# Optimization experiments

Measured on AMD Instinct MI355X. Metric: run time of the kernel, lower is better.

## Reference

```python
import jax, jax.numpy as jnp
import numpy as np

BOUND = 1.0
MIN_NEAR = 0.2
T_THRESH = 1e-4
MAX_STEPS = 128


def _near_far(rays_o, rays_d):
    # ray-AABB intersection with [-BOUND, BOUND]^3 (near_far_from_aabb)
    d = jnp.where(jnp.abs(rays_d) < 1e-9, 1e-9, rays_d)
    t1 = (-BOUND - rays_o) / d
    t2 = (BOUND - rays_o) / d
    near = jnp.max(jnp.minimum(t1, t2), axis=-1)
    far = jnp.min(jnp.maximum(t1, t2), axis=-1)
    near = jnp.maximum(near, MIN_NEAR)
    far = jnp.maximum(far, near)
    return near, far


def _sample_triplane(planes, pts):
    # planes: [3, C, RES, RES]; pts: [N, 3] in [-1, 1] -> feats [N, 3C]
    def bil(plane, uv):
        res = plane.shape[-1]
        xy = (uv + 1.0) * 0.5 * (res - 1)
        x0 = jnp.clip(jnp.floor(xy).astype(jnp.int32), 0, res - 2)
        w = xy - x0
        wx, wy = w[:, 0], w[:, 1]
        xi, yi = x0[:, 0], x0[:, 1]
        f00 = plane[:, yi, xi]
        f01 = plane[:, yi, xi + 1]
        f10 = plane[:, yi + 1, xi]
        f11 = plane[:, yi + 1, xi + 1]
        f = (f00 * (1 - wx) * (1 - wy) + f01 * wx * (1 - wy)
             + f10 * (1 - wx) * wy + f11 * wx * wy)
        return f.T  # [N, C]
    uvs = (pts[:, jnp.array([0, 1])], pts[:, jnp.array([0, 2])], pts[:, jnp.array([1, 2])])
    return jnp.concatenate([bil(planes[p], uvs[p]) for p in range(3)], axis=-1)


def _forward(rays_o, rays_d, code, density_grid, grid_size, W1, b1, W2, b2, W3, b3):
    S, R, _ = rays_o.shape
    K = MAX_STEPS
    near, far = _near_far(rays_o, rays_d)
    t = (jnp.arange(K, dtype=rays_o.dtype) + 0.5) / K
    z = near[..., None] + (far - near)[..., None] * t            # [S,R,K]
    delta = (far - near) / K                                     # [S,R]
    xyz = rays_o[:, :, None, :] + rays_d[:, :, None, :] * z[..., None]
    xyz = jnp.clip(xyz, -BOUND, BOUND)                           # [S,R,K,3]
    # occupancy-grid masking (density bitfield lookup)
    idx = jnp.clip(((xyz + BOUND) / (2 * BOUND) * grid_size).astype(jnp.int32), 0, grid_size - 1)
    occ = jax.vmap(lambda g, i: g[i[..., 0], i[..., 1], i[..., 2]])(density_grid, idx) > 0  # [S,R,K]
    # point decode: triplane features + small MLP -> (sigma, rgb)
    pts = (xyz / BOUND).reshape(S, R * K, 3)
    feats = jax.vmap(_sample_triplane)(code, pts)                # [S,R*K,96]
    h = jax.nn.relu(feats @ W1 + b1)
    h = jax.nn.relu(h @ W2 + b2)
    out = h @ W3 + b3
    sigma = jax.nn.softplus(out[..., 0]).reshape(S, R, K) * occ.astype(rays_o.dtype)
    rgb = jax.nn.sigmoid(out[..., 1:]).reshape(S, R, K, 3)
    # alpha compositing with early termination at T_thresh
    tau = sigma * delta[..., None]
    T = jnp.exp(-jnp.concatenate([jnp.zeros_like(tau[..., :1]), jnp.cumsum(tau, axis=-1)[..., :-1]], axis=-1))
    alpha = 1.0 - jnp.exp(-tau)
    w = jnp.where(T > T_THRESH, alpha * T, 0.0)
    weights_sum = w.sum(-1)                                      # [S,R]
    depth = (w * z).sum(-1)                                      # [S,R]
    image = (w[..., None] * rgb).sum(-2)                         # [S,R,3]
    return weights_sum, depth, image


def setup_inputs():
    key = jax.random.key(0)
    ks = jax.random.split(key, 8)
    S, R, C, RES, G, H = 4, 2048, 32, 128, 128, 128
    o = jax.random.normal(ks[0], (S, R, 3), jnp.float32)
    rays_o = o / (jnp.linalg.norm(o, axis=-1, keepdims=True) + 1e-6) * 2.5
    d = -rays_o + 0.3 * jax.random.normal(ks[1], (S, R, 3), jnp.float32)
    rays_d = d / (jnp.linalg.norm(d, axis=-1, keepdims=True) + 1e-6)
    code = 0.1 * jax.random.normal(ks[2], (S, 3, C, RES, RES), jnp.float32)
    density_grid = jnp.ones((S, G, G, G), jnp.int32)
    din = 3 * C
    W1 = jax.random.normal(ks[3], (din, H), jnp.float32) / np.sqrt(din).astype(np.float32)
    b1 = jnp.zeros((H,), jnp.float32)
    W2 = jax.random.normal(ks[4], (H, H), jnp.float32) / np.sqrt(H).astype(np.float32)
    b2 = jnp.zeros((H,), jnp.float32)
    W3 = jax.random.normal(ks[5], (H, 4), jnp.float32) / np.sqrt(H).astype(np.float32)
    b3 = jnp.zeros((4,), jnp.float32)
    return {"rays_o": rays_o, "rays_d": rays_d, "code": code, "density_grid": density_grid,
            "grid_size": G, "W1": W1, "b1": b1, "W2": W2, "b2": b2, "W3": W3, "b3": b3}


def reference(rays_o, rays_d, code, density_grid, grid_size, W1, b1, W2, b2, W3, b3):
    return _forward(rays_o, rays_d, code, density_grid, grid_size, W1, b1, W2, b2, W3, b3)
```

## Files before the change

### kernel.cpp

```cpp
#include <hip/hip_runtime.h>
#include <math.h>

#define S_ 4
#define R_ 2048
#define K_ 128
#define C_ 32
#define RES_ 128
#define G_ 128
#define H_ 128

typedef __bf16 bf16x8 __attribute__((ext_vector_type(8)));
typedef float f32x4 __attribute__((ext_vector_type(4)));
typedef float f32x2 __attribute__((ext_vector_type(2)));
typedef unsigned short u16x8 __attribute__((ext_vector_type(8)));

#define CODET_OFF 0
#define CODET_SZ  (S_*3*RES_*RES_*C_/2)
#define W1F_OFF   (CODET_OFF + CODET_SZ)
#define W1F_SZ    (128*96/2)
#define W2F_OFF   (W1F_OFF + W1F_SZ)
#define W2F_SZ    (128*128/2)
#define GB_OFF    (W2F_OFF + W2F_SZ)
#define GB_SZ     (S_*G_*G_*G_/32)
#define SR_OFF    (GB_OFF + GB_SZ)

#define ROWP 136

__device__ __forceinline__ unsigned short f2bf(float x) {
  unsigned int u = __float_as_uint(x);
  unsigned int r = u + 0x7fffu + ((u >> 16) & 1u);
  return (unsigned short)(r >> 16);
}

__global__ __launch_bounds__(256) void k_pre(
    const float* __restrict__ src, unsigned short* __restrict__ dst,
    const int* __restrict__ dgrid, unsigned int* __restrict__ gbits,
    const float* __restrict__ W1, const float* __restrict__ W2,
    unsigned short* __restrict__ W1F, unsigned short* __restrict__ W2F) {
  __shared__ float tile[32 * 65];
  const int t = threadIdx.x;
  const int b = blockIdx.x;
  if (b < 3072) {
    const int slab = b >> 8;
    const int xy0 = (b & 255) << 6;
    const float* sp = src + slab * (C_ * RES_ * RES_);
    unsigned short* dp = dst + slab * (RES_ * RES_ * C_);
    const int i = t & 63, cg = t >> 6;
#pragma unroll
    for (int j = 0; j < 8; ++j) {
      int c = cg * 8 + j;
      tile[c * 65 + i] = sp[c * (RES_ * RES_) + xy0 + i];
    }
    __syncthreads();
    const int i2 = t >> 2, sub = t & 3;
    u16x8 pk;
#pragma unroll
    for (int j = 0; j < 8; ++j) pk[j] = f2bf(tile[(sub * 8 + j) * 65 + i2]);
    *(u16x8*)(dp + (xy0 + i2) * C_ + sub * 8) = pk;
  } else if (b < 4096) {
    const int base0 = (b - 3072) * 8192;
    const int lane = t & 63;
#pragma unroll 4
    for (int j = 0; j < 32; ++j) {
      const int idx = base0 + j * 256 + t;
      const unsigned long long m = __ballot(dgrid[idx] > 0);
      if (lane == 0)
        gbits[idx >> 5] = (unsigned int)m;
      else if (lane == 32)
        gbits[idx >> 5] = (unsigned int)(m >> 32);
    }
  } else {
    const int slice = b - 4096;
    for (int i = slice * 256 + t; i < 128 * 96; i += 16 * 256) {
      const int j = i & 7, lane = (i >> 3) & 63, fi = i >> 9;
      const int nt = fi / 3, kt = fi - 3 * nt;
      const int k = kt * 32 + (lane >> 4) * 8 + j;
      const int n = nt * 16 + (lane & 15);
      W1F[i] = f2bf(W1[k * H_ + n]);
    }
    for (int i = slice * 256 + t; i < 128 * 128; i += 16 * 256) {
      const int j = i & 7, lane = (i >> 3) & 63, fi = i >> 9;
      const int nt = fi >> 2, kt = fi & 3;
      const int k = kt * 32 + (lane >> 4) * 8 + j;
      const int n = nt * 16 + (lane & 15);
      W2F[i] = f2bf(W2[k * H_ + n]);
    }
  }
}

__device__ __forceinline__ void near_far(float ox, float oy, float oz,
                                         float dx, float dy, float dz,
                                         float& nearv, float& farv) {
  float ddx = fabsf(dx) < 1e-9f ? 1e-9f : dx;
  float ddy = fabsf(dy) < 1e-9f ? 1e-9f : dy;
  float ddz = fabsf(dz) < 1e-9f ? 1e-9f : dz;
  float ix = 1.f / ddx, iy = 1.f / ddy, iz = 1.f / ddz;
  float t1x = (-1.f - ox) * ix, t2x = (1.f - ox) * ix;
  float t1y = (-1.f - oy) * iy, t2y = (1.f - oy) * iy;
  float t1z = (-1.f - oz) * iz, t2z = (1.f - oz) * iz;
  float mnx = fminf(t1x, t2x), mxx = fmaxf(t1x, t2x);
  float mny = fminf(t1y, t2y), mxy = fmaxf(t1y, t2y);
  float mnz = fminf(t1z, t2z), mxz = fmaxf(t1z, t2z);
  nearv = fmaxf(fmaxf(fmaxf(mnx, mny), mnz), 0.2f);
  farv = fmaxf(fminf(fminf(mxx, mxy), mxz), nearv);
}

__device__ __forceinline__ float reduce16(const float (&part)[4][4], const int ln) {
  float v16[16];
#pragma unroll
  for (int rr = 0; rr < 4; ++rr)
#pragma unroll
    for (int qq = 0; qq < 4; ++qq) v16[rr * 4 + qq] = part[rr][qq];
  float v8[8];
#pragma unroll
  for (int j = 0; j < 8; ++j) {
    const float a = v16[2 * j], c = v16[2 * j + 1];
    const float send = (ln & 1) ? a : c;
    const float keep = (ln & 1) ? c : a;
    v8[j] = keep + __shfl_xor(send, 1);
  }
  float v4a[4];
#pragma unroll
  for (int j = 0; j < 4; ++j) {
    const float a = v8[2 * j], c = v8[2 * j + 1];
    const float send = (ln & 2) ? a : c;
    const float keep = (ln & 2) ? c : a;
    v4a[j] = keep + __shfl_xor(send, 2);
  }
  float v2a[2];
#pragma unroll
  for (int j = 0; j < 2; ++j) {
    const float a = v4a[2 * j], c = v4a[2 * j + 1];
    const float send = (ln & 4) ? a : c;
    const float keep = (ln & 4) ? c : a;
    v2a[j] = keep + __shfl_xor(send, 4);
  }
  const float a = v2a[0], c = v2a[1];
  const float send = (ln & 8) ? a : c;
  const float keep = (ln & 8) ? c : a;
  return keep + __shfl_xor(send, 8);
}

__global__ __launch_bounds__(256, 4) void k_fused(
    const float* __restrict__ rays_o, const float* __restrict__ rays_d,
    const unsigned short* __restrict__ codeT, const unsigned int* __restrict__ gbits,
    const unsigned short* __restrict__ W1F, const float* __restrict__ b1,
    const unsigned short* __restrict__ W2F, const float* __restrict__ b2,
    const float* __restrict__ W3, const float* __restrict__ b3,
    float* __restrict__ sr) {
  __shared__ __align__(16) unsigned short smem[128 * ROWP];
  unsigned short* fA = smem;
  unsigned short* h1s = smem;

  const int t = threadIdx.x;
  const int w = t >> 6, lane = t & 63;
  const int quad = lane >> 4, ln = lane & 15;
  const int p = t >> 1, q = t & 1;
  const int ray = blockIdx.x;
  const int s = ray >> 11;
  const int pG0 = ray * K_;

  const float* ob = rays_o + ray * 3;
  const float* db = rays_d + ray * 3;
  const float ox = ob[0], oy = ob[1], oz = ob[2];
  const float dx = db[0], dy = db[1], dz = db[2];
  float nearv, farv;
  near_far(ox, oy, oz, dx, dy, dz, nearv, farv);

  const int q_s = ln & 3, rr_s = ln >> 2;
  const int m_o0 = 32 * w + quad * 4 + rr_s;
  const int m_o1 = m_o0 + 16;
  unsigned int occw0, occw1;
  int occb0, occb1;
  {
    const float zm = nearv + (farv - nearv) * ((m_o0 + 0.5f) * (1.0f / K_));
    const float pxm = fminf(fmaxf(ox + dx * zm, -1.f), 1.f);
    const float pym = fminf(fmaxf(oy + dy * zm, -1.f), 1.f);
    const float pzm = fminf(fmaxf(oz + dz * zm, -1.f), 1.f);
    const int i0 = min((int)((pxm + 1.f) * 64.f), G_ - 1);
    const int i1 = min((int)((pym + 1.f) * 64.f), G_ - 1);
    const int i2 = min((int)((pzm + 1.f) * 64.f), G_ - 1);
    const int bidx = ((s * G_ + i0) * G_ + i1) * G_ + i2;
    occw0 = gbits[bidx >> 5];
    occb0 = bidx & 31;
  }
  {
    const float zm = nearv + (farv - nearv) * ((m_o1 + 0.5f) * (1.0f / K_));
    const float pxm = fminf(fmaxf(ox + dx * zm, -1.f), 1.f);
    const float pym = fminf(fmaxf(oy + dy * zm, -1.f), 1.f);
    const float pzm = fminf(fmaxf(oz + dz * zm, -1.f), 1.f);
    const int i0 = min((int)((pxm + 1.f) * 64.f), G_ - 1);
    const int i1 = min((int)((pym + 1.f) * 64.f), G_ - 1);
    const int i2 = min((int)((pzm + 1.f) * 64.f), G_ - 1);
    const int bidx = ((s * G_ + i0) * G_ + i1) * G_ + i2;
    occw1 = gbits[bidx >> 5];
    occb1 = bidx & 31;
  }

  const float zs = nearv + (farv - nearv) * ((p + 0.5f) * (1.0f / K_));
  const float px = fminf(fmaxf(ox + dx * zs, -1.f), 1.f);
  const float py = fminf(fmaxf(oy + dy * zs, -1.f), 1.f);
  const float pz = fminf(fmaxf(oz + dz * zs, -1.f), 1.f);

  float w00a, w01a, w10a, w11a, w00b, w01b, w10b, w11b, w00c, w01c, w10c, w11c;
  int off0, off1, off2;
  {
    float fx = (px + 1.f) * 0.5f * 127.f, fy = (py + 1.f) * 0.5f * 127.f;
    int xi = min((int)fx, RES_ - 2), yi = min((int)fy, RES_ - 2);
    float wx = fx - (float)xi, wy = fy - (float)yi;
    w00a = (1.f - wx) * (1.f - wy); w01a = wx * (1.f - wy);
    w10a = (1.f - wx) * wy;         w11a = wx * wy;
    off0 = ((s * 3 + 0) * (RES_ * RES_) + yi * RES_ + xi) * C_;
  }
  {
    float fx = (px + 1.f) * 0.5f * 127.f, fy = (pz + 1.f) * 0.5f * 127.f;
    int xi = min((int)fx, RES_ - 2), yi = min((int)fy, RES_ - 2);
    float wx = fx - (float)xi, wy = fy - (float)yi;
    w00b = (1.f - wx) * (1.f - wy); w01b = wx * (1.f - wy);
    w10b = (1.f - wx) * wy;         w11b = wx * wy;
    off1 = ((s * 3 + 1) * (RES_ * RES_) + yi * RES_ + xi) * C_;
  }
  {
    float fx = (py + 1.f) * 0.5f * 127.f, fy = (pz + 1.f) * 0.5f * 127.f;
    int xi = min((int)fx, RES_ - 2), yi = min((int)fy, RES_ - 2);
    float wx = fx - (float)xi, wy = fy - (float)yi;
    w00c = (1.f - wx) * (1.f - wy); w01c = wx * (1.f - wy);
    w10c = (1.f - wx) * wy;         w11c = wx * wy;
    off2 = ((s * 3 + 2) * (RES_ * RES_) + yi * RES_ + xi) * C_;
  }

#pragma unroll
  for (int u = 0; u < 6; ++u) {
    const int f = 48 * q + 8 * u;
    const int pl = f >> 5;
    const int c = f & 31;
    const int off = (pl == 0) ? off0 : ((pl == 1) ? off1 : off2);
    const float W00 = (pl == 0) ? w00a : ((pl == 1) ? w00b : w00c);
    const float W01 = (pl == 0) ? w01a : ((pl == 1) ? w01b : w01c);
    const float W10 = (pl == 0) ? w10a : ((pl == 1) ? w10b : w10c);
    const float W11 = (pl == 0) ? w11a : ((pl == 1) ? w11b : w11c);
    const unsigned short* bp = codeT + off + c;
    const uint4 A = *(const uint4*)(bp);
    const uint4 B = *(const uint4*)(bp + C_);
    const uint4 Cv = *(const uint4*)(bp + RES_ * C_);
    const uint4 D = *(const uint4*)(bp + RES_ * C_ + C_);
    const unsigned int aw[4] = {A.x, A.y, A.z, A.w};
    const unsigned int bw[4] = {B.x, B.y, B.z, B.w};
    const unsigned int cw[4] = {Cv.x, Cv.y, Cv.z, Cv.w};
    const unsigned int dw[4] = {D.x, D.y, D.z, D.w};
    const f32x2 W00v = {W00, W00}, W01v = {W01, W01}, W10v = {W10, W10}, W11v = {W11, W11};
    unsigned int ow[4];
#pragma unroll
    for (int e2 = 0; e2 < 4; ++e2) {
      const f32x2 va = {__uint_as_float(aw[e2] << 16), __uint_as_float(aw[e2] & 0xffff0000u)};
      const f32x2 vb = {__uint_as_float(bw[e2] << 16), __uint_as_float(bw[e2] & 0xffff0000u)};
      const f32x2 vc = {__uint_as_float(cw[e2] << 16), __uint_as_float(cw[e2] & 0xffff0000u)};
      const f32x2 vd = {__uint_as_float(dw[e2] << 16), __uint_as_float(dw[e2] & 0xffff0000u)};
      const f32x2 fv = W00v * va + W01v * vb + W10v * vc + W11v * vd;
      ow[e2] = __builtin_amdgcn_perm(__float_as_uint(fv[1]), __float_as_uint(fv[0]),
                                     0x07060302u);
    }
    *(uint4*)(fA + p * ROWP + f) = make_uint4(ow[0], ow[1], ow[2], ow[3]);
  }

  const int rowA = 32 * w + ln;
  const int rowB = rowA + 16;

  {
    bf16x8 aA[3], aB[3];
#pragma unroll
    for (int kt = 0; kt < 3; ++kt) {
      aA[kt] = *(const bf16x8*)(fA + rowA * ROWP + kt * 32 + quad * 8);
      aB[kt] = *(const bf16x8*)(fA + rowB * ROWP + kt * 32 + quad * 8);
    }
#pragma unroll
    for (int nt = 0; nt < 8; ++nt) {
      const bf16x8 b0 = *(const bf16x8*)(W1F + ((nt * 3 + 0) * 64 + lane) * 8);
      const bf16x8 b1v = *(const bf16x8*)(W1F + ((nt * 3 + 1) * 64 + lane) * 8);
      const bf16x8 b2v = *(const bf16x8*)(W1F + ((nt * 3 + 2) * 64 + lane) * 8);
      f32x4 accA = {0.f, 0.f, 0.f, 0.f};
      f32x4 accB = {0.f, 0.f, 0.f, 0.f};
      accA = __builtin_amdgcn_mfma_f32_16x16x32_bf16(aA[0], b0, accA, 0, 0, 0);
      accB = __builtin_amdgcn_mfma_f32_16x16x32_bf16(aB[0], b0, accB, 0, 0, 0);
      accA = __builtin_amdgcn_mfma_f32_16x16x32_bf16(aA[1], b1v, accA, 0, 0, 0);
      accB = __builtin_amdgcn_mfma_f32_16x16x32_bf16(aB[1], b1v, accB, 0, 0, 0);
      accA = __builtin_amdgcn_mfma_f32_16x16x32_bf16(aA[2], b2v, accA, 0, 0, 0);
      accB = __builtin_amdgcn_mfma_f32_16x16x32_bf16(aB[2], b2v, accB, 0, 0, 0);
      const int n = nt * 16 + ln;
      const float bias = b1[n];
#pragma unroll
      for (int rr = 0; rr < 4; ++rr) {
        const int mA = 32 * w + quad * 4 + rr;
        const float vA = fmaxf(accA[rr] + bias, 0.f);
        h1s[mA * ROWP + n] = (unsigned short)(__float_as_uint(vA) >> 16);
        const float vB = fmaxf(accB[rr] + bias, 0.f);
        h1s[(mA + 16) * ROWP + n] = (unsigned short)(__float_as_uint(vB) >> 16);
      }
    }
  }

  float part0[4][4], part1[4][4];
#pragma unroll
  for (int rr = 0; rr < 4; ++rr)
#pragma unroll
    for (int qq = 0; qq < 4; ++qq) {
      part0[rr][qq] = 0.f;
      part1[rr][qq] = 0.f;
    }
  {
    bf16x8 aA[4], aB[4];
#pragma unroll
    for (int kt = 0; kt < 4; ++kt) {
      aA[kt] = *(const bf16x8*)(h1s + rowA * ROWP + kt * 32 + quad * 8);
      aB[kt] = *(const bf16x8*)(h1s + rowB * ROWP + kt * 32 + quad * 8);
    }
#pragma unroll
    for (int nt = 0; nt < 8; ++nt) {
      const bf16x8 b0 = *(const bf16x8*)(W2F + ((nt * 4 + 0) * 64 + lane) * 8);
      const bf16x8 b1v = *(const bf16x8*)(W2F + ((nt * 4 + 1) * 64 + lane) * 8);
      const bf16x8 b2v = *(const bf16x8*)(W2F + ((nt * 4 + 2) * 64 + lane) * 8);
      const bf16x8 b3v = *(const bf16x8*)(W2F + ((nt * 4 + 3) * 64 + lane) * 8);
      f32x4 accA = {0.f, 0.f, 0.f, 0.f};
      f32x4 accB = {0.f, 0.f, 0.f, 0.f};
      accA = __builtin_amdgcn_mfma_f32_16x16x32_bf16(aA[0], b0, accA, 0, 0, 0);
      accB = __builtin_amdgcn_mfma_f32_16x16x32_bf16(aB[0], b0, accB, 0, 0, 0);
      accA = __builtin_amdgcn_mfma_f32_16x16x32_bf16(aA[1], b1v, accA, 0, 0, 0);
      accB = __builtin_amdgcn_mfma_f32_16x16x32_bf16(aB[1], b1v, accB, 0, 0, 0);
      accA = __builtin_amdgcn_mfma_f32_16x16x32_bf16(aA[2], b2v, accA, 0, 0, 0);
      accB = __builtin_amdgcn_mfma_f32_16x16x32_bf16(aB[2], b2v, accB, 0, 0, 0);
      accA = __builtin_amdgcn_mfma_f32_16x16x32_bf16(aA[3], b3v, accA, 0, 0, 0);
      accB = __builtin_amdgcn_mfma_f32_16x16x32_bf16(aB[3], b3v, accB, 0, 0, 0);
      const int n = nt * 16 + ln;
      const float b2n = b2[n];
      const float4 w3v = *(const float4*)(W3 + n * 4);
#pragma unroll
      for (int rr = 0; rr < 4; ++rr) {
        const float hA = fmaxf(accA[rr] + b2n, 0.f);
        part0[rr][0] = fmaf(hA, w3v.x, part0[rr][0]);
        part0[rr][1] = fmaf(hA, w3v.y, part0[rr][1]);
        part0[rr][2] = fmaf(hA, w3v.z, part0[rr][2]);
        part0[rr][3] = fmaf(hA, w3v.w, part0[rr][3]);
        const float hB = fmaxf(accB[rr] + b2n, 0.f);
        part1[rr][0] = fmaf(hB, w3v.x, part1[rr][0]);
        part1[rr][1] = fmaf(hB, w3v.y, part1[rr][1]);
        part1[rr][2] = fmaf(hB, w3v.z, part1[rr][2]);
        part1[rr][3] = fmaf(hB, w3v.w, part1[rr][3]);
      }
    }
  }

  const float bq = b3[q_s];
  {
    const float val = reduce16(part0, ln) + bq;
    float outv;
    if (q_s == 0) {
      const int occ = (occw0 >> occb0) & 1;
      const float sp = val > 20.f ? val : log1pf(expf(val));
      outv = occ ? sp : 0.f;
    } else {
      outv = 1.f / (1.f + expf(-val));
    }
    sr[(pG0 + m_o0) * 4 + q_s] = outv;
  }
  {
    const float val = reduce16(part1, ln) + bq;
    float outv;
    if (q_s == 0) {
      const int occ = (occw1 >> occb1) & 1;
      const float sp = val > 20.f ? val : log1pf(expf(val));
      outv = occ ? sp : 0.f;
    } else {
      outv = 1.f / (1.f + expf(-val));
    }
    sr[(pG0 + m_o1) * 4 + q_s] = outv;
  }
}

__global__ __launch_bounds__(256) void k_render(
    const float* __restrict__ rays_o, const float* __restrict__ rays_d,
    const float4* __restrict__ sr4, float* __restrict__ out) {
  const int lane = threadIdx.x & 63;
  const int ray = blockIdx.x * 4 + (threadIdx.x >> 6);
  const int s = ray >> 11, r = ray & (R_ - 1);
  const float* ob = rays_o + (s * R_ + r) * 3;
  const float* db = rays_d + (s * R_ + r) * 3;
  float nearv, farv;
  near_far(ob[0], ob[1], ob[2], db[0], db[1], db[2], nearv, farv);
  const float delta = (farv - nearv) * (1.0f / K_);

  const int k0 = lane * 2;
  const float4 A = sr4[ray * K_ + k0];
  const float4 B = sr4[ray * K_ + k0 + 1];
  const float tau0 = A.x * delta, tau1 = B.x * delta;
  const float local = tau0 + tau1;
  float scan = local;
#pragma unroll
  for (int off = 1; off < 64; off <<= 1) {
    const float vsh = __shfl_up(scan, off);
    if (lane >= off) scan += vsh;
  }
  const float pre = scan - local;
  const float T0 = expf(-pre);
  const float T1 = expf(-(pre + tau0));
  const float a0 = 1.f - expf(-tau0);
  const float a1 = 1.f - expf(-tau1);
  const float w0 = (T0 > 1e-4f) ? a0 * T0 : 0.f;
  const float w1 = (T1 > 1e-4f) ? a1 * T1 : 0.f;
  const float z0 = nearv + (farv - nearv) * ((k0 + 0.5f) * (1.f / K_));
  const float z1 = nearv + (farv - nearv) * ((k0 + 1.5f) * (1.f / K_));

  float sw = w0 + w1;
  float sd = w0 * z0 + w1 * z1;
  float sred = w0 * A.y + w1 * B.y;
  float sgrn = w0 * A.z + w1 * B.z;
  float sblu = w0 * A.w + w1 * B.w;
#pragma unroll
  for (int mk = 32; mk >= 1; mk >>= 1) {
    sw += __shfl_xor(sw, mk);
    sd += __shfl_xor(sd, mk);
    sred += __shfl_xor(sred, mk);
    sgrn += __shfl_xor(sgrn, mk);
    sblu += __shfl_xor(sblu, mk);
  }
  if (lane == 0) {
    out[ray] = sw;
    out[S_ * R_ + ray] = sd;
    out[2 * S_ * R_ + ray * 3 + 0] = sred;
    out[2 * S_ * R_ + ray * 3 + 1] = sgrn;
    out[2 * S_ * R_ + ray * 3 + 2] = sblu;
  }
}

extern "C" void kernel_launch(void* const* d_in, const int* in_sizes, int n_in,
                              void* d_out, int out_size, void* d_ws, size_t ws_size,
                              hipStream_t stream) {
  const float* rays_o = (const float*)d_in[0];
  const float* rays_d = (const float*)d_in[1];
  const float* code = (const float*)d_in[2];
  const int* dgrid = (const int*)d_in[3];
  const float* W1 = (const float*)d_in[5];
  const float* b1 = (const float*)d_in[6];
  const float* W2 = (const float*)d_in[7];
  const float* b2 = (const float*)d_in[8];
  const float* W3 = (const float*)d_in[9];
  const float* b3 = (const float*)d_in[10];

  float* ws = (float*)d_ws;
  unsigned short* codeT = (unsigned short*)(ws + CODET_OFF);
  unsigned short* W1F = (unsigned short*)(ws + W1F_OFF);
  unsigned short* W2F = (unsigned short*)(ws + W2F_OFF);
  unsigned int* gbits = (unsigned int*)(ws + GB_OFF);
  float* sr = ws + SR_OFF;

  hipLaunchKernelGGL(k_pre, dim3(4112), dim3(256), 0, stream,
                     code, codeT, dgrid, gbits, W1, W2, W1F, W2F);
  hipLaunchKernelGGL(k_fused, dim3(S_ * R_), dim3(256), 0, stream,
                     rays_o, rays_d, codeT, gbits, W1F, b1, W2F, b2, W3, b3, sr);
  hipLaunchKernelGGL(k_render, dim3((S_ * R_) / 4), dim3(256), 0, stream,
                     rays_o, rays_d, (const float4*)sr, (float*)d_out);
}
```

Before: 282.3 us.

## Swizzle LDS layout, raise occupancy, prefetch W1 tile, pack layer-3 FMAs

Replaces the padded LDS rows (stride 136) with an XOR-swizzled 128-wide layout. This shrinks shared memory per block and avoids bank conflicts on the MFMA operand reads. Launch bounds rise from 4 to 5 blocks per SM to increase occupancy. The first W1 fragment is now loaded early to hide its global latency, and the layer-3 dot products use packed f32x2 FMAs. The tighter register budget risks spills.

```diff
diff --git a/kernel.cpp b/kernel.cpp
--- a/kernel.cpp
+++ b/kernel.cpp
@@ -24,7 +24,7 @@
 #define GB_SZ     (S_*G_*G_*G_/32)
 #define SR_OFF    (GB_OFF + GB_SZ)
 
-#define ROWP 136
+#define SWZ(row, col) (((row) << 7) + ((col) ^ (((row) & 15) << 3)))
 
 __device__ __forceinline__ unsigned short f2bf(float x) {
   unsigned int u = __float_as_uint(x);
@@ -105,12 +105,14 @@
   farv = fmaxf(fminf(fminf(mxx, mxy), mxz), nearv);
 }
 
-__device__ __forceinline__ float reduce16(const float (&part)[4][4], const int ln) {
+__device__ __forceinline__ float reduce16p(const f32x2 (&part)[2][4], const int ln) {
   float v16[16];
 #pragma unroll
-  for (int rr = 0; rr < 4; ++rr)
-#pragma unroll
-    for (int qq = 0; qq < 4; ++qq) v16[rr * 4 + qq] = part[rr][qq];
+  for (int pr = 0; pr < 2; ++pr)
+#pragma unroll
+    for (int e = 0; e < 2; ++e)
+#pragma unroll
+      for (int qq = 0; qq < 4; ++qq) v16[(2 * pr + e) * 4 + qq] = part[pr][qq][e];
   float v8[8];
 #pragma unroll
   for (int j = 0; j < 8; ++j) {
@@ -141,14 +143,14 @@
   return keep + __shfl_xor(send, 8);
 }
 
-__global__ __launch_bounds__(256, 4) void k_fused(
+__global__ __launch_bounds__(256, 5) void k_fused(
     const float* __restrict__ rays_o, const float* __restrict__ rays_d,
     const unsigned short* __restrict__ codeT, const unsigned int* __restrict__ gbits,
     const unsigned short* __restrict__ W1F, const float* __restrict__ b1,
     const unsigned short* __restrict__ W2F, const float* __restrict__ b2,
     const float* __restrict__ W3, const float* __restrict__ b3,
     float* __restrict__ sr) {
-  __shared__ __align__(16) unsigned short smem[128 * ROWP];
+  __shared__ __align__(16) unsigned short smem[128 * 128];
   unsigned short* fA = smem;
   unsigned short* h1s = smem;
 
@@ -159,6 +161,10 @@
   const int ray = blockIdx.x;
   const int s = ray >> 11;
   const int pG0 = ray * K_;
+
+  const bf16x8 pb0 = *(const bf16x8*)(W1F + ((0 * 3 + 0) * 64 + lane) * 8);
+  const bf16x8 pb1 = *(const bf16x8*)(W1F + ((0 * 3 + 1) * 64 + lane) * 8);
+  const bf16x8 pb2 = *(const bf16x8*)(W1F + ((0 * 3 + 2) * 64 + lane) * 8);
 
   const float* ob = rays_o + ray * 3;
   const float* db = rays_d + ray * 3;
@@ -260,28 +266,27 @@
       ow[e2] = __builtin_amdgcn_perm(__float_as_uint(fv[1]), __float_as_uint(fv[0]),
                                      0x07060302u);
     }
-    *(uint4*)(fA + p * ROWP + f) = make_uint4(ow[0], ow[1], ow[2], ow[3]);
+    *(uint4*)(fA + SWZ(p, f)) = make_uint4(ow[0], ow[1], ow[2], ow[3]);
   }
 
   const int rowA = 32 * w + ln;
   const int rowB = rowA + 16;
+  const f32x4 kz = {0.f, 0.f, 0.f, 0.f};
 
   {
     bf16x8 aA[3], aB[3];
 #pragma unroll
     for (int kt = 0; kt < 3; ++kt) {
-      aA[kt] = *(const bf16x8*)(fA + rowA * ROWP + kt * 32 + quad * 8);
-      aB[kt] = *(const bf16x8*)(fA + rowB * ROWP + kt * 32 + quad * 8);
+      aA[kt] = *(const bf16x8*)(fA + SWZ(rowA, kt * 32 + quad * 8));
+      aB[kt] = *(const bf16x8*)(fA + SWZ(rowB, kt * 32 + quad * 8));
     }
 #pragma unroll
     for (int nt = 0; nt < 8; ++nt) {
-      const bf16x8 b0 = *(const bf16x8*)(W1F + ((nt * 3 + 0) * 64 + lane) * 8);
-      const bf16x8 b1v = *(const bf16x8*)(W1F + ((nt * 3 + 1) * 64 + lane) * 8);
-      const bf16x8 b2v = *(const bf16x8*)(W1F + ((nt * 3 + 2) * 64 + lane) * 8);
-      f32x4 accA = {0.f, 0.f, 0.f, 0.f};
-      f32x4 accB = {0.f, 0.f, 0.f, 0.f};
-      accA = __builtin_amdgcn_mfma_f32_16x16x32_bf16(aA[0], b0, accA, 0, 0, 0);
-      accB = __builtin_amdgcn_mfma_f32_16x16x32_bf16(aB[0], b0, accB, 0, 0, 0);
+      const bf16x8 b0 = (nt == 0) ? pb0 : *(const bf16x8*)(W1F + ((nt * 3 + 0) * 64 + lane) * 8);
+      const bf16x8 b1v = (nt == 0) ? pb1 : *(const bf16x8*)(W1F + ((nt * 3 + 1) * 64 + lane) * 8);
+      const bf16x8 b2v = (nt == 0) ? pb2 : *(const bf16x8*)(W1F + ((nt * 3 + 2) * 64 + lane) * 8);
+      f32x4 accA = __builtin_amdgcn_mfma_f32_16x16x32_bf16(aA[0], b0, kz, 0, 0, 0);
+      f32x4 accB = __builtin_amdgcn_mfma_f32_16x16x32_bf16(aB[0], b0, kz, 0, 0, 0);
       accA = __builtin_amdgcn_mfma_f32_16x16x32_bf16(aA[1], b1v, accA, 0, 0, 0);
       accB = __builtin_amdgcn_mfma_f32_16x16x32_bf16(aB[1], b1v, accB, 0, 0, 0);
       accA = __builtin_amdgcn_mfma_f32_16x16x32_bf16(aA[2], b2v, accA, 0, 0, 0);
@@ -292,27 +297,27 @@
       for (int rr = 0; rr < 4; ++rr) {
         const int mA = 32 * w + quad * 4 + rr;
         const float vA = fmaxf(accA[rr] + bias, 0.f);
-        h1s[mA * ROWP + n] = (unsigned short)(__float_as_uint(vA) >> 16);
+        h1s[SWZ(mA, n)] = (unsigned short)(__float_as_uint(vA) >> 16);
         const float vB = fmaxf(accB[rr] + bias, 0.f);
-        h1s[(mA + 16) * ROWP + n] = (unsigned short)(__float_as_uint(vB) >> 16);
+        h1s[SWZ(mA + 16, n)] = (unsigned short)(__float_as_uint(vB) >> 16);
       }
     }
   }
 
-  float part0[4][4], part1[4][4];
-#pragma unroll
-  for (int rr = 0; rr < 4; ++rr)
+  f32x2 p0[2][4], p1[2][4];
+#pragma unroll
+  for (int pr = 0; pr < 2; ++pr)
 #pragma unroll
     for (int qq = 0; qq < 4; ++qq) {
-      part0[rr][qq] = 0.f;
-      part1[rr][qq] = 0.f;
+      p0[pr][qq] = (f32x2){0.f, 0.f};
+      p1[pr][qq] = (f32x2){0.f, 0.f};
     }
   {
     bf16x8 aA[4], aB[4];
 #pragma unroll
     for (int kt = 0; kt < 4; ++kt) {
-      aA[kt] = *(const bf16x8*)(h1s + rowA * ROWP + kt * 32 + quad * 8);
-      aB[kt] = *(const bf16x8*)(h1s + rowB * ROWP + kt * 32 + quad * 8);
+      aA[kt] = *(const bf16x8*)(h1s + SWZ(rowA, kt * 32 + quad * 8));
+      aB[kt] = *(const bf16x8*)(h1s + SWZ(rowB, kt * 32 + quad * 8));
     }
 #pragma unroll
     for (int nt = 0; nt < 8; ++nt) {
@@ -320,10 +325,8 @@
       const bf16x8 b1v = *(const bf16x8*)(W2F + ((nt * 4 + 1) * 64 + lane) * 8);
       const bf16x8 b2v = *(const bf16x8*)(W2F + ((nt * 4 + 2) * 64 + lane) * 8);
       const bf16x8 b3v = *(const bf16x8*)(W2F + ((nt * 4 + 3) * 64 + lane) * 8);
-      f32x4 accA = {0.f, 0.f, 0.f, 0.f};
-      f32x4 accB = {0.f, 0.f, 0.f, 0.f};
-      accA = __builtin_amdgcn_mfma_f32_16x16x32_bf16(aA[0], b0, accA, 0, 0, 0);
-      accB = __builtin_amdgcn_mfma_f32_16x16x32_bf16(aB[0], b0, accB, 0, 0, 0);
+      f32x4 accA = __builtin_amdgcn_mfma_f32_16x16x32_bf16(aA[0], b0, kz, 0, 0, 0);
+      f32x4 accB = __builtin_amdgcn_mfma_f32_16x16x32_bf16(aB[0], b0, kz, 0, 0, 0);
       accA = __builtin_amdgcn_mfma_f32_16x16x32_bf16(aA[1], b1v, accA, 0, 0, 0);
       accB = __builtin_amdgcn_mfma_f32_16x16x32_bf16(aB[1], b1v, accB, 0, 0, 0);
       accA = __builtin_amdgcn_mfma_f32_16x16x32_bf16(aA[2], b2v, accA, 0, 0, 0);
@@ -333,25 +336,26 @@
       const int n = nt * 16 + ln;
       const float b2n = b2[n];
       const float4 w3v = *(const float4*)(W3 + n * 4);
-#pragma unroll
-      for (int rr = 0; rr < 4; ++rr) {
-        const float hA = fmaxf(accA[rr] + b2n, 0.f);
-        part0[rr][0] = fmaf(hA, w3v.x, part0[rr][0]);
-        part0[rr][1] = fmaf(hA, w3v.y, part0[rr][1]);
-        part0[rr][2] = fmaf(hA, w3v.z, part0[rr][2]);
-        part0[rr][3] = fmaf(hA, w3v.w, part0[rr][3]);
-        const float hB = fmaxf(accB[rr] + b2n, 0.f);
-        part1[rr][0] = fmaf(hB, w3v.x, part1[rr][0]);
-        part1[rr][1] = fmaf(hB, w3v.y, part1[rr][1]);
-        part1[rr][2] = fmaf(hB, w3v.z, part1[rr][2]);
-        part1[rr][3] = fmaf(hB, w3v.w, part1[rr][3]);
+      const f32x2 wxv = {w3v.x, w3v.x}, wyv = {w3v.y, w3v.y};
+      const f32x2 wzv = {w3v.z, w3v.z}, wwv = {w3v.w, w3v.w};
+#pragma unroll
+      for (int pr = 0; pr < 2; ++pr) {
+        f32x2 hA, hB;
+        hA[0] = fmaxf(accA[2 * pr] + b2n, 0.f);
+        hA[1] = fmaxf(accA[2 * pr + 1] + b2n, 0.f);
+        hB[0] = fmaxf(accB[2 * pr] + b2n, 0.f);
+        hB[1] = fmaxf(accB[2 * pr + 1] + b2n, 0.f);
+        p0[pr][0] += hA * wxv;  p0[pr][1] += hA * wyv;
+        p0[pr][2] += hA * wzv;  p0[pr][3] += hA * wwv;
+        p1[pr][0] += hB * wxv;  p1[pr][1] += hB * wyv;
+        p1[pr][2] += hB * wzv;  p1[pr][3] += hB * wwv;
       }
     }
   }
 
   const float bq = b3[q_s];
   {
-    const float val = reduce16(part0, ln) + bq;
+    const float val = reduce16p(p0, ln) + bq;
     float outv;
     if (q_s == 0) {
       const int occ = (occw0 >> occb0) & 1;
@@ -363,7 +367,7 @@
     sr[(pG0 + m_o0) * 4 + q_s] = outv;
   }
   {
-    const float val = reduce16(part1, ln) + bq;
+    const float val = reduce16p(p1, ln) + bq;
     float outv;
     if (q_s == 0) {
       const int occ = (occw1 >> occb1) & 1;
```

Result: slower. 455.7 us (+61.4%).
